# Performance work log

Measured on AMD Instinct MI355X. Metric: run time of the kernel, lower is better.

The kernel has to match this reference:

```python
import jax, jax.numpy as jnp
import numpy as np

B, S, F, O = 128, 8, 32, 16  # batch, board_size, in_features, out_features
D = 2 * S - 1                # diff_size = 15 relative offsets per axis


def setup_inputs() -> dict:
    key = jax.random.key(0)
    k1, k2, k3 = jax.random.split(key, 3)
    inp = jax.random.normal(k1, (B, S, S, F), dtype=jnp.float32)
    # torch.nn.Bilinear init: U(-1/sqrt(in1_features), 1/sqrt(in1_features))
    bound = 1.0 / np.sqrt(F)
    W = jax.random.uniform(k2, (D, D, O, F, F), jnp.float32, -bound, bound)
    b = jax.random.uniform(k3, (D, D, O), jnp.float32, -bound, bound)
    return {"inp": inp, "W": W, "b": b}


def reference(inp, W, b):
    # inp: (B, S, S, F); W: (D, D, O, F, F); b: (D, D, O)
    s = inp.shape[1]
    idx = jnp.arange(s)
    # offset index: off[a, bb] = bb - a + (s - 1), in [0, 2s-2]
    off = idx[None, :] - idx[:, None] + (s - 1)  # (S, S)
    # gather per-pair bilinear weights: Wg[ax, bx, ay, by] = W[bx-ax+7, by-ay+7]
    Wg = W[off[:, :, None, None], off[None, None, :, :]]  # (S,S,S,S,O,F,F)
    bg = b[off[:, :, None, None], off[None, None, :, :]]  # (S,S,S,S,O) [ax,bx,ay,by]
    # out[b, ax, ay, bx, by, o] = a_i W_oij b_j + bias_o
    out = jnp.einsum('bxyi,xXyYoij,bXYj->bxyXYo', inp, Wg, inp)
    out = out + bg.transpose(0, 2, 1, 3, 4)[None]  # bias to [ax,ay,bx,by,o]
    return out
```

## Files before the change

kernel.cpp:

```cpp
#include <hip/hip_runtime.h>

typedef _Float16 f16;
typedef _Float16 f16x8 __attribute__((ext_vector_type(8)));
typedef float f32x4 __attribute__((ext_vector_type(4)));
typedef unsigned int u32;
typedef const __attribute__((address_space(1))) u32* gas1_t;
typedef __attribute__((address_space(3))) u32* las3_t;

#define WGRAN 460800
#define IGRAN 32768

__global__ __launch_bounds__(256) void convert_kernel(
    const float* __restrict__ W, const float* __restrict__ inp,
    f16* __restrict__ W_h, f16* __restrict__ inp_h)
{
    const int g = blockIdx.x * 256 + threadIdx.x;
    if (g < WGRAN) {
        const int dxdy = g >> 11;
        const int r = g & 2047;
        const int i = r >> 6, o = (r >> 2) & 15, quad = r & 3;
        const float* src = W + (size_t)dxdy * 16384 + o * 1024 + i * 32 + quad * 8;
        const float4 v0 = *(const float4*)src;
        const float4 v1 = *(const float4*)(src + 4);
        f16x8 h = { (f16)v0.x, (f16)v0.y, (f16)v0.z, (f16)v0.w,
                    (f16)v1.x, (f16)v1.y, (f16)v1.z, (f16)v1.w };
        *(f16x8*)(W_h + (size_t)g * 8) = h;
    } else {
        const int k = g - WGRAN;
        const float* src = inp + (size_t)k * 8;
        const float4 v0 = *(const float4*)src;
        const float4 v1 = *(const float4*)(src + 4);
        f16x8 h = { (f16)v0.x, (f16)v0.y, (f16)v0.z, (f16)v0.w,
                    (f16)v1.x, (f16)v1.y, (f16)v1.z, (f16)v1.w };
        *(f16x8*)(inp_h + (size_t)k * 8) = h;
    }
}

__global__ __launch_bounds__(256, 5) void rel_mfma3(
    const f16* __restrict__ W_h,
    const f16* __restrict__ inp_h,
    const float* __restrict__ bias,
    float* __restrict__ out)
{
    extern __shared__ __align__(16) f16 Wl[];

    const int bid = blockIdx.x;
    const int Y = bid & 7, X = (bid >> 3) & 7, y = (bid >> 6) & 7, x = (bid >> 9) & 7;
    const int dx = X - x + 7, dy = Y - y + 7;
    const int dxdy = dx * 15 + dy;

    const int t = threadIdx.x;

    {
        const f16* base = W_h + (size_t)dxdy * 16384;
        #pragma unroll
        for (int it = 0; it < 8; ++it) {
            const int idx = (it * 256 + t) * 8;
            __builtin_amdgcn_global_load_lds((gas1_t)(base + idx),
                                             (las3_t)&Wl[idx], 16, 0, 0);
        }
    }

    const int lane = t & 63;
    const int wave = t >> 6;
    const int quad = lane >> 4;
    const int m = lane & 15;

    f16x8 a0[4], a1[4], c0, c1;
    {
        const int b0 = wave * 32 + m;
        const int b1 = b0 + 16;
        const f16* ar0 = inp_h + ((b0 * 8 + x) * 8 + y) * 32;
        const f16* ar1 = inp_h + ((b1 * 8 + x) * 8 + y) * 32;
        #pragma unroll
        for (int g = 0; g < 4; ++g) {
            a0[g] = *(const f16x8*)(ar0 + g * 8);
            a1[g] = *(const f16x8*)(ar1 + g * 8);
        }
        c0 = *(const f16x8*)(inp_h + ((b0 * 8 + X) * 8 + Y) * 32 + quad * 8);
        c1 = *(const f16x8*)(inp_h + ((b1 * 8 + X) * 8 + Y) * 32 + quad * 8);
    }

    __syncthreads();

    f32x4 acc0 = {0.f, 0.f, 0.f, 0.f};
    f32x4 acc1 = {0.f, 0.f, 0.f, 0.f};
    const f16* wl = &Wl[m * 32 + quad * 8];
    f16x8 bfrag = *(const f16x8*)(wl);
    #pragma unroll
    for (int kb = 0; kb < 32; ++kb) {
        const f16x8 bcur = bfrag;
        if (kb < 31)
            bfrag = *(const f16x8*)(wl + (kb + 1) * 512);
        const f16 av0 = a0[kb >> 3][kb & 7];
        const f16 av1 = a1[kb >> 3][kb & 7];
        const f16x8 af0 = c0 * av0;
        const f16x8 af1 = c1 * av1;
        acc0 = __builtin_amdgcn_mfma_f32_16x16x32_f16(af0, bcur, acc0, 0, 0, 0);
        acc1 = __builtin_amdgcn_mfma_f32_16x16x32_f16(af1, bcur, acc1, 0, 0, 0);
    }

    const float bv = bias[dxdy * 16 + m];
    #pragma unroll
    for (int r = 0; r < 4; ++r) {
        const int b0 = wave * 32 + quad * 4 + r;
        const int b1 = b0 + 16;
        out[((size_t)b0 * 4096 + bid) * 16 + m] = acc0[r] + bv;
        out[((size_t)b1 * 4096 + bid) * 16 + m] = acc1[r] + bv;
    }
}

extern "C" void kernel_launch(void* const* d_in, const int* in_sizes, int n_in,
                              void* d_out, int out_size, void* d_ws, size_t ws_size,
                              hipStream_t stream)
{
    const float* inp  = (const float*)d_in[0];
    const float* W    = (const float*)d_in[1];
    const float* bias = (const float*)d_in[2];
    float* out = (float*)d_out;

    f16* W_h   = (f16*)d_ws;
    f16* inp_h = (f16*)d_ws + (size_t)WGRAN * 8;

    hipLaunchKernelGGL(convert_kernel, dim3((WGRAN + IGRAN) / 256), dim3(256), 0,
                       stream, W, inp, W_h, inp_h);
    hipLaunchKernelGGL(rel_mfma3, dim3(4096), dim3(256), 32768, stream,
                       W_h, inp_h, bias, out);
}
```

Measured before the change: 104.6 us.

## Split K across wave pairs and reduce partial sums through LDS

Each wave now covers four 16-row batch tiles over half of the 32 K-steps, where before it covered two tiles over all 32. Each loaded W fragment is reused across four MFMAs, which halves the LDS B-fragment reads per wave. The partial accumulators from the two K halves are summed through shared memory before bias is added and the output is stored. This adds an extra barrier, an LDS round trip, and more registers for the four accumulators and the A/C fragments, which could hurt occupancy.

Result: slower. 108.5 us (+3.7%).

```diff
diff --git a/kernel.cpp b/kernel.cpp
--- a/kernel.cpp
+++ b/kernel.cpp
@@ -36,7 +36,7 @@
     }
 }
 
-__global__ __launch_bounds__(256, 5) void rel_mfma3(
+__global__ __launch_bounds__(256, 5) void rel_mfma4(
     const f16* __restrict__ W_h,
     const f16* __restrict__ inp_h,
     const float* __restrict__ bias,
@@ -63,50 +63,57 @@
 
     const int lane = t & 63;
     const int wave = t >> 6;
+    const int wset = wave & 1;
+    const int khalf = wave >> 1;
     const int quad = lane >> 4;
     const int m = lane & 15;
 
-    f16x8 a0[4], a1[4], c0, c1;
-    {
-        const int b0 = wave * 32 + m;
-        const int b1 = b0 + 16;
-        const f16* ar0 = inp_h + ((b0 * 8 + x) * 8 + y) * 32;
-        const f16* ar1 = inp_h + ((b1 * 8 + x) * 8 + y) * 32;
-        #pragma unroll
-        for (int g = 0; g < 4; ++g) {
-            a0[g] = *(const f16x8*)(ar0 + g * 8);
-            a1[g] = *(const f16x8*)(ar1 + g * 8);
-        }
-        c0 = *(const f16x8*)(inp_h + ((b0 * 8 + X) * 8 + Y) * 32 + quad * 8);
-        c1 = *(const f16x8*)(inp_h + ((b1 * 8 + X) * 8 + Y) * 32 + quad * 8);
+    f16x8 a[4][2], c[4];
+    #pragma unroll
+    for (int tt = 0; tt < 4; ++tt) {
+        const int b0 = (wset * 4 + tt) * 16 + m;
+        const f16* ar = inp_h + ((b0 * 8 + x) * 8 + y) * 32 + khalf * 16;
+        a[tt][0] = *(const f16x8*)(ar);
+        a[tt][1] = *(const f16x8*)(ar + 8);
+        c[tt] = *(const f16x8*)(inp_h + ((b0 * 8 + X) * 8 + Y) * 32 + quad * 8);
     }
 
     __syncthreads();
 
-    f32x4 acc0 = {0.f, 0.f, 0.f, 0.f};
-    f32x4 acc1 = {0.f, 0.f, 0.f, 0.f};
-    const f16* wl = &Wl[m * 32 + quad * 8];
+    f32x4 acc[4] = { {0,0,0,0}, {0,0,0,0}, {0,0,0,0}, {0,0,0,0} };
+    const f16* wl = &Wl[khalf * 16 * 512 + m * 32 + quad * 8];
     f16x8 bfrag = *(const f16x8*)(wl);
     #pragma unroll
-    for (int kb = 0; kb < 32; ++kb) {
+    for (int kbl = 0; kbl < 16; ++kbl) {
         const f16x8 bcur = bfrag;
-        if (kb < 31)
-            bfrag = *(const f16x8*)(wl + (kb + 1) * 512);
-        const f16 av0 = a0[kb >> 3][kb & 7];
-        const f16 av1 = a1[kb >> 3][kb & 7];
-        const f16x8 af0 = c0 * av0;
-        const f16x8 af1 = c1 * av1;
-        acc0 = __builtin_amdgcn_mfma_f32_16x16x32_f16(af0, bcur, acc0, 0, 0, 0);
-        acc1 = __builtin_amdgcn_mfma_f32_16x16x32_f16(af1, bcur, acc1, 0, 0, 0);
+        if (kbl < 15)
+            bfrag = *(const f16x8*)(wl + (kbl + 1) * 512);
+        #pragma unroll
+        for (int tt = 0; tt < 4; ++tt) {
+            const f16x8 af = c[tt] * a[tt][kbl >> 3][kbl & 7];
+            acc[tt] = __builtin_amdgcn_mfma_f32_16x16x32_f16(af, bcur, acc[tt], 0, 0, 0);
+        }
     }
 
-    const float bv = bias[dxdy * 16 + m];
-    #pragma unroll
-    for (int r = 0; r < 4; ++r) {
-        const int b0 = wave * 32 + quad * 4 + r;
-        const int b1 = b0 + 16;
-        out[((size_t)b0 * 4096 + bid) * 16 + m] = acc0[r] + bv;
-        out[((size_t)b1 * 4096 + bid) * 16 + m] = acc1[r] + bv;
+    __syncthreads();
+    float* xbuf = (float*)Wl;
+    if (khalf == 1) {
+        #pragma unroll
+        for (int tt = 0; tt < 4; ++tt)
+            *(f32x4*)(&xbuf[(wset * 64 + lane) * 16 + tt * 4]) = acc[tt];
+    }
+    __syncthreads();
+    if (khalf == 0) {
+        const float bv = bias[dxdy * 16 + m];
+        #pragma unroll
+        for (int tt = 0; tt < 4; ++tt) {
+            const f32x4 part = *(const f32x4*)(&xbuf[(wset * 64 + lane) * 16 + tt * 4]);
+            #pragma unroll
+            for (int r = 0; r < 4; ++r) {
+                const int b = (wset * 4 + tt) * 16 + quad * 4 + r;
+                out[((size_t)b * 4096 + bid) * 16 + m] = acc[tt][r] + part[r] + bv;
+            }
+        }
     }
 }
 
@@ -124,6 +131,6 @@
 
     hipLaunchKernelGGL(convert_kernel, dim3((WGRAN + IGRAN) / 256), dim3(256), 0,
                        stream, W, inp, W_h, inp_h);
-    hipLaunchKernelGGL(rel_mfma3, dim3(4096), dim3(256), 32768, stream,
+    hipLaunchKernelGGL(rel_mfma4, dim3(4096), dim3(256), 32768, stream,
                        W_h, inp_h, bias, out);
 }
```
